# Performance work log

Hardware: AMD Instinct MI355X
Metric: run time of the kernel (lower is better)

The kernel has to match this reference:

```python
import jax, jax.numpy as jnp
import numpy as np

B, C, H, W = 512, 64, 32, 64
NUM_NODE = 128


def setup_inputs() -> dict:
    key = jax.random.key(0)
    ks = jax.random.split(key, 11)
    f = jnp.float32
    def nrm(k, shape, s):
        return jax.random.normal(k, shape, f) * s
    return {
        "x":   jax.random.normal(ks[0], (B, C, H, W), f),
        "w11": nrm(ks[1], (32, 64, 1, 1), 0.1), "b11": nrm(ks[2], (32,), 0.05),
        "w12": nrm(ks[3], (16, 32, 3, 3), 0.1), "b12": nrm(ks[4], (16,), 0.05),
        "w21": nrm(ks[5], (8, 16, 1, 1), 0.1),  "b21": nrm(ks[6], (8,), 0.05),
        "w22": nrm(ks[7], (4, 8, 3, 3), 0.1),   "b22": nrm(ks[8], (4,), 0.05),
        "fcw": nrm(ks[9], (2 * NUM_NODE, 32 * 64 * 4), 0.05),
        "fcb": nrm(ks[10], (2 * NUM_NODE,), 0.05),
    }


def _conv_relu(x, w, b, pad):
    y = jax.lax.conv_general_dilated(
        x, w, window_strides=(1, 1), padding=[(pad, pad), (pad, pad)],
        dimension_numbers=("NCHW", "OIHW", "NCHW"))
    return jax.nn.relu(y + b[None, :, None, None])


def reference(x, w11, b11, w12, b12, w21, b21, w22, b22, fcw, fcb):
    # --- GraphGen3: conv stack -> fc -> n_Sigmoid -> [B, N, 2] ---
    h = _conv_relu(x, w11, b11, 0)
    h = _conv_relu(h, w12, b12, 1)
    h = _conv_relu(h, w21, b21, 0)
    h = _conv_relu(h, w22, b22, 1)          # [B, 4, 32, 64]
    z = h.reshape(h.shape[0], -1) @ fcw.T + fcb  # [B, 2N]
    c01 = jax.nn.sigmoid(3.0 * z).reshape(x.shape[0], -1, 2)  # n_Sigmoid(x, 3)
    # --- get_coord: scale normalized coords to pixel range ---
    Hd, Wd = x.shape[2], x.shape[3]
    coord = c01 * jnp.array([Hd - 1, Wd - 1], x.dtype)  # [B, N, 2]
    # --- th_batch_map_coordinates: clamp, corner gather, bilinear lerp ---
    ch = jnp.clip(coord[..., 0], 0.0, Hd - 1)
    cw = jnp.clip(coord[..., 1], 0.0, Wd - 1)
    h0 = jnp.floor(ch).astype(jnp.int32); h1 = jnp.ceil(ch).astype(jnp.int32)
    w0 = jnp.floor(cw).astype(jnp.int32); w1 = jnp.ceil(cw).astype(jnp.int32)
    bidx = jnp.arange(x.shape[0])[:, None]  # [B, 1]
    def gv(hi, wi):
        return x[bidx, :, hi, wi]           # gather -> [B, N, C]
    v_lt = gv(h0, w0); v_rt = gv(h1, w0)
    v_lb = gv(h0, w1); v_rb = gv(h1, w1)
    oh = (ch - h0.astype(x.dtype))[..., None]
    ow = (cw - w0.astype(x.dtype))[..., None]
    vt = v_lt + oh * (v_rt - v_lt)
    vb = v_lb + oh * (v_rb - v_lb)
    graph_feat = vt + ow * (vb - vt)        # [B, N, C] (matches permute(0,2,1))
    return graph_feat, coord
```

## Files before the change

kernel.cpp:

```cpp
#include <hip/hip_runtime.h>
#include <hip/hip_fp16.h>
#include <cstdint>

#define BATCH 512
#define CIN   64
#define HH    32
#define WW    64
#define HW    2048
#define C1    32
#define C2    16
#define C3    8
#define C4    4
#define NOUT  256
#define KFC   8192
#define NODES 128
#define KS    16
#define GF_SIZE (BATCH * NODES * CIN)

typedef __attribute__((ext_vector_type(8))) short bfrag;
typedef __attribute__((ext_vector_type(4))) float ffrag;

__device__ __forceinline__ ushort bf_trunc(float f) { return (ushort)(__float_as_uint(f) >> 16); }
__device__ __forceinline__ float  bf_truncf(float f) { return __uint_as_float(__float_as_uint(f) & 0xffff0000u); }
__device__ __forceinline__ ushort f2bf(float f) {
  uint32_t u = __float_as_uint(f);
  return (ushort)((u + 0x7fffu + ((u >> 16) & 1u)) >> 16);
}
__device__ __forceinline__ uint32_t pack2(float a, float b) {
  return (uint32_t)f2bf(a) | ((uint32_t)f2bf(b) << 16);
}
__device__ __forceinline__ uint32_t packhi2(float a, float b) {
  return (uint32_t)bf_trunc(a) | ((uint32_t)bf_trunc(b) << 16);
}
__device__ __forceinline__ ushort f2h(float f) { return __half_as_ushort(__float2half_rn(f)); }
__device__ __forceinline__ uint32_t packh2(float a, float b) {
  return (uint32_t)f2h(a) | ((uint32_t)f2h(b) << 16);
}
__device__ __forceinline__ float h2f(uint32_t u) { return __half2float(__ushort_as_half((ushort)u)); }
__device__ __forceinline__ float bf2f(ushort u) { return __uint_as_float(((uint32_t)u) << 16); }

__global__ __launch_bounds__(256) void k_xpose(
    const float* __restrict__ x, ushort* __restrict__ xt)
{
  __shared__ uint32_t tb[256 * 33];
  const int t  = threadIdx.x;
  const int b  = blockIdx.y;
  const int rg = blockIdx.x;
  const float* xp = x + (size_t)b * CIN * HW + rg * 256 + t;
  #pragma unroll
  for (int j = 0; j < 32; ++j) {
    float v0 = xp[(size_t)(2 * j) * HW];
    float v1 = xp[(size_t)(2 * j + 1) * HW];
    tb[t * 33 + j] = pack2(v0, v1);
  }
  __syncthreads();
  ushort* op = xt + ((size_t)b * HW + rg * 256) * CIN;
  #pragma unroll
  for (int k = 0; k < 8; ++k) {
    const int u = k * 256 + t;
    const int p = u >> 3, q = u & 7;
    uint4 v;
    v.x = tb[p * 33 + q * 4 + 0];
    v.y = tb[p * 33 + q * 4 + 1];
    v.z = tb[p * 33 + q * 4 + 2];
    v.w = tb[p * 33 + q * 4 + 3];
    *(uint4*)(op + (size_t)u * 8) = v;
  }
}

__global__ __launch_bounds__(256) void k_conv1234(
    const ushort* __restrict__ xt, const float* __restrict__ w11, const float* __restrict__ b11,
    const float* __restrict__ w12, const float* __restrict__ b12,
    const float* __restrict__ w21, const float* __restrict__ b21,
    const float* __restrict__ w22, const float* __restrict__ b22,
    ushort* __restrict__ h4h, ushort* __restrict__ h4l, int b0)
{
  __shared__ __align__(16) char smem[12 * 66 * 64];
  const int tid = threadIdx.x;
  const int l   = tid & 63;
  const int wv  = tid >> 6;
  const int lr  = l & 15;
  const int lg  = l >> 4;
  const int r0  = blockIdx.x * 8;
  const int bg  = b0 + blockIdx.y;
  const ushort* xtb = xt + (size_t)bg * HW * CIN;

  if (tid < 192) {
    int cell = tid >> 3, q = tid & 7;
    int row = cell >> 1, colb = (cell & 1) ? 65 : 0;
    *(uint2*)(smem + ((row * 66 + colb) << 6) + q * 8) = uint2{0u, 0u};
  }

  bfrag w1h[2][2], w1l[2][2];
  #pragma unroll
  for (int m = 0; m < 2; ++m) {
    #pragma unroll
    for (int ks = 0; ks < 2; ++ks) {
      const float* wp = w11 + (m * 16 + lr) * 64 + ks * 32 + lg * 8;
      #pragma unroll
      for (int e = 0; e < 8; ++e) {
        float v = wp[e];
        w1h[m][ks][e] = (short)bf_trunc(v);
        w1l[m][ks][e] = (short)f2bf(v - bf_truncf(v));
      }
    }
  }
  float bias1[2][4];
  #pragma unroll
  for (int m = 0; m < 2; ++m) {
    #pragma unroll
    for (int r = 0; r < 4; ++r) bias1[m][r] = b11[m * 16 + lg * 4 + r];
  }

  auto ldfrag = [&](int nt, bfrag& f0, bfrag& f1) {
    const int ry = nt >> 2, col0 = (nt & 3) << 4;
    const int y  = r0 - 2 + ry;
    if (y >= 0 && y < HH) {
      const ushort* xp = xtb + (size_t)(y * WW + col0 + lr) * CIN + lg * 8;
      f0 = *(const bfrag*)xp;
      f1 = *(const bfrag*)(xp + 32);
    } else {
      #pragma unroll
      for (int e = 0; e < 8; ++e) { f0[e] = 0; f1[e] = 0; }
    }
  };
  auto comp = [&](int nt, bfrag f0, bfrag f1) {
    const int ry = nt >> 2, col0 = (nt & 3) << 4;
    const int y  = r0 - 2 + ry;
    const bool valid = (y >= 0) && (y < HH);
    const int colb = col0 + 1 + lr;
    ffrag a0 = {0.f, 0.f, 0.f, 0.f}, a1 = {0.f, 0.f, 0.f, 0.f};
    a0 = __builtin_amdgcn_mfma_f32_16x16x32_bf16(w1h[0][0], f0, a0, 0, 0, 0);
    a0 = __builtin_amdgcn_mfma_f32_16x16x32_bf16(w1l[0][0], f0, a0, 0, 0, 0);
    a0 = __builtin_amdgcn_mfma_f32_16x16x32_bf16(w1h[0][1], f1, a0, 0, 0, 0);
    a0 = __builtin_amdgcn_mfma_f32_16x16x32_bf16(w1l[0][1], f1, a0, 0, 0, 0);
    a1 = __builtin_amdgcn_mfma_f32_16x16x32_bf16(w1h[1][0], f0, a1, 0, 0, 0);
    a1 = __builtin_amdgcn_mfma_f32_16x16x32_bf16(w1l[1][0], f0, a1, 0, 0, 0);
    a1 = __builtin_amdgcn_mfma_f32_16x16x32_bf16(w1h[1][1], f1, a1, 0, 0, 0);
    a1 = __builtin_amdgcn_mfma_f32_16x16x32_bf16(w1l[1][1], f1, a1, 0, 0, 0);
    #pragma unroll
    for (int m = 0; m < 2; ++m) {
      uint2 sv;
      if (valid) {
        float v0 = fmaxf((m ? a1[0] : a0[0]) + bias1[m][0], 0.f);
        float v1 = fmaxf((m ? a1[1] : a0[1]) + bias1[m][1], 0.f);
        float v2 = fmaxf((m ? a1[2] : a0[2]) + bias1[m][2], 0.f);
        float v3 = fmaxf((m ? a1[3] : a0[3]) + bias1[m][3], 0.f);
        sv = uint2{pack2(v0, v1), pack2(v2, v3)};
      } else {
        sv = uint2{0u, 0u};
      }
      int chunk = (m * 2 + (lg >> 1)) ^ ((colb >> 1) & 3);
      char* dst = smem + ((ry * 66 + colb) << 6) + (chunk << 4) + (lg & 1) * 8;
      *(uint2*)dst = sv;
    }
  };

  {
    bfrag c0, c1, n0, n1;
    ldfrag(wv * 12 + 0, c0, c1);
    #pragma unroll
    for (int i = 0; i < 12; ++i) {
      if (i < 11) ldfrag(wv * 12 + i + 1, n0, n1);
      comp(wv * 12 + i, c0, c1);
      c0 = n0; c1 = n1;
    }
  }
  __syncthreads();

  bfrag w2h[9], w2l[9];
  #pragma unroll
  for (int t = 0; t < 9; ++t) {
    const float* wp = w12 + lr * 288 + t;
    #pragma unroll
    for (int e = 0; e < 8; ++e) {
      float v = wp[(lg * 8 + e) * 9];
      w2h[t][e] = (short)bf_trunc(v);
      w2l[t][e] = (short)f2bf(v - bf_truncf(v));
    }
  }
  float bias2[4];
  #pragma unroll
  for (int r = 0; r < 4; ++r) bias2[r] = b12[lg * 4 + r];

  uint32_t ph0[10], ph1[10];
  #pragma unroll
  for (int i = 0; i < 10; ++i) {
    const int nt   = wv * 10 + i;
    const int hryo = nt >> 2;
    const int col0 = (nt & 3) << 4;
    ffrag acc = {0.f, 0.f, 0.f, 0.f};
    #pragma unroll
    for (int ky = 0; ky < 3; ++ky) {
      const int row = hryo + ky;
      #pragma unroll
      for (int kx = 0; kx < 3; ++kx) {
        const int colb  = col0 + lr + kx;
        const int chunk = lg ^ ((colb >> 1) & 3);
        const bfrag hv = *(const bfrag*)(smem + ((row * 66 + colb) << 6) + (chunk << 4));
        acc = __builtin_amdgcn_mfma_f32_16x16x32_bf16(w2h[ky * 3 + kx], hv, acc, 0, 0, 0);
        acc = __builtin_amdgcn_mfma_f32_16x16x32_bf16(w2l[ky * 3 + kx], hv, acc, 0, 0, 0);
      }
    }
    ph0[i] = packh2(fmaxf(acc[0] + bias2[0], 0.f), fmaxf(acc[1] + bias2[1], 0.f));
    ph1[i] = packh2(fmaxf(acc[2] + bias2[2], 0.f), fmaxf(acc[3] + bias2[3], 0.f));
  }
  __syncthreads();

  #pragma unroll
  for (int i = 0; i < 10; ++i) {
    const int nt   = wv * 10 + i;
    const int hryo = nt >> 2;
    const int col  = ((nt & 3) << 4) + lr;
    *(uint2*)(smem + ((hryo * 64 + col) << 5) + lg * 8) = uint2{ph0[i], ph1[i]};
  }
  __syncthreads();

  float* h3b = (float*)(smem + 20480);
  for (int p = tid; p < 640; p += 256) {
    const int ry = p >> 6, wc = p & 63;
    const int y  = r0 - 1 + ry;
    float* hd = h3b + (ry * 64 + wc) * 9;
    if (y >= 0 && y < HH) {
      const uint4 ua = *(const uint4*)(smem + ((ry * 64 + wc) << 5));
      const uint4 ub = *(const uint4*)(smem + ((ry * 64 + wc) << 5) + 16);
      uint32_t uw[8] = {ua.x, ua.y, ua.z, ua.w, ub.x, ub.y, ub.z, ub.w};
      float xv[16];
      #pragma unroll
      for (int j = 0; j < 8; ++j) {
        xv[2*j]   = h2f(uw[j] & 0xffffu);
        xv[2*j+1] = h2f(uw[j] >> 16);
      }
      float acc[C3];
      #pragma unroll
      for (int o = 0; o < C3; ++o) acc[o] = b21[o];
      #pragma unroll
      for (int c = 0; c < 16; ++c) {
        float v = xv[c];
        #pragma unroll
        for (int o = 0; o < C3; ++o)
          acc[o] = fmaf(v, w21[o * 16 + c], acc[o]);
      }
      #pragma unroll
      for (int c = 0; c < C3; ++c) hd[c] = fmaxf(acc[c], 0.f);
    } else {
      #pragma unroll
      for (int c = 0; c < C3; ++c) hd[c] = 0.f;
    }
  }
  __syncthreads();

  for (int p = tid; p < 512; p += 256) {
    const int yl = p >> 6, wc = p & 63;
    float acc[C4] = {b22[0], b22[1], b22[2], b22[3]};
    #pragma unroll
    for (int ky = 0; ky < 3; ++ky) {
      #pragma unroll
      for (int kx = 0; kx < 3; ++kx) {
        const int wcc = wc + kx - 1;
        if (wcc < 0 || wcc >= WW) continue;
        const float* hb = h3b + ((yl + ky) * 64 + wcc) * 9;
        const int tap = ky * 3 + kx;
        #pragma unroll
        for (int c = 0; c < C3; ++c) {
          float v = hb[c];
          #pragma unroll
          for (int o = 0; o < C4; ++o)
            acc[o] = fmaf(v, w22[(o * 8 + c) * 9 + tap], acc[o]);
        }
      }
    }
    const size_t base = (size_t)blockIdx.y * KFC + (r0 + yl) * WW + wc;
    #pragma unroll
    for (int o = 0; o < C4; ++o) {
      float v = fmaxf(acc[o], 0.f);
      h4h[base + (size_t)o * HW] = bf_trunc(v);
      h4l[base + (size_t)o * HW] = f2bf(v - bf_truncf(v));
    }
  }
}

__global__ __launch_bounds__(256) void k_cvt_fcw(
    const float* __restrict__ w, ushort* __restrict__ hi, ushort* __restrict__ lo)
{
  const int i = (blockIdx.x * 256 + threadIdx.x) * 8;
  const float4 a = *(const float4*)(w + i);
  const float4 b = *(const float4*)(w + i + 4);
  uint4 hv, lv;
  hv.x = packhi2(a.x, a.y); hv.y = packhi2(a.z, a.w);
  hv.z = packhi2(b.x, b.y); hv.w = packhi2(b.z, b.w);
  lv.x = pack2(a.x - bf_truncf(a.x), a.y - bf_truncf(a.y));
  lv.y = pack2(a.z - bf_truncf(a.z), a.w - bf_truncf(a.w));
  lv.z = pack2(b.x - bf_truncf(b.x), b.y - bf_truncf(b.y));
  lv.w = pack2(b.z - bf_truncf(b.z), b.w - bf_truncf(b.w));
  *(uint4*)(hi + i) = hv;
  *(uint4*)(lo + i) = lv;
}

__global__ __launch_bounds__(256) void k_fc(
    const ushort* __restrict__ Ahp, const ushort* __restrict__ Alp,
    const ushort* __restrict__ Bhp, const ushort* __restrict__ Blp,
    float* __restrict__ zpart, int cb)
{
  const int tid = threadIdx.x;
  const int l   = tid & 63;
  const int wv  = tid >> 6;
  const int lr  = l & 15;
  const int lg  = l >> 4;
  const int m0  = blockIdx.x * 64 + (wv >> 1) * 32;
  const int n0  = blockIdx.y * 64 + (wv & 1) * 32;
  const int k0  = blockIdx.z * (KFC / KS);

  int mrow[2], nrow[2];
  #pragma unroll
  for (int t = 0; t < 2; ++t) {
    int m = m0 + t * 16 + lr;
    mrow[t] = m < cb ? m : cb - 1;
    nrow[t] = n0 + t * 16 + lr;
  }
  ffrag acc[2][2] = {};

  #pragma unroll 1
  for (int kc = 0; kc < (KFC / KS) / 32; ++kc) {
    const int k = k0 + kc * 32 + lg * 8;
    bfrag ah[2], al[2], bh[2], bl[2];
    #pragma unroll
    for (int t = 0; t < 2; ++t) {
      ah[t] = *(const bfrag*)(Ahp + (size_t)mrow[t] * KFC + k);
      al[t] = *(const bfrag*)(Alp + (size_t)mrow[t] * KFC + k);
      bh[t] = *(const bfrag*)(Bhp + (size_t)nrow[t] * KFC + k);
      bl[t] = *(const bfrag*)(Blp + (size_t)nrow[t] * KFC + k);
    }
    #pragma unroll
    for (int mt = 0; mt < 2; ++mt) {
      #pragma unroll
      for (int nt = 0; nt < 2; ++nt) {
        acc[mt][nt] = __builtin_amdgcn_mfma_f32_16x16x32_bf16(ah[mt], bh[nt], acc[mt][nt], 0, 0, 0);
        acc[mt][nt] = __builtin_amdgcn_mfma_f32_16x16x32_bf16(ah[mt], bl[nt], acc[mt][nt], 0, 0, 0);
        acc[mt][nt] = __builtin_amdgcn_mfma_f32_16x16x32_bf16(al[mt], bh[nt], acc[mt][nt], 0, 0, 0);
      }
    }
  }

  #pragma unroll
  for (int mt = 0; mt < 2; ++mt) {
    #pragma unroll
    for (int r = 0; r < 4; ++r) {
      const int m = m0 + mt * 16 + lg * 4 + r;
      if (m < cb) {
        #pragma unroll
        for (int nt = 0; nt < 2; ++nt)
          zpart[((size_t)blockIdx.z * cb + m) * NOUT + n0 + nt * 16 + lr] = acc[mt][nt][r];
      }
    }
  }
}

__global__ __launch_bounds__(256) void k_gather(
    const ushort* __restrict__ xt, const float* __restrict__ zpart,
    const float* __restrict__ fcb, float* __restrict__ out, int cb, int b0)
{
  const int bid = blockIdx.x;
  int bl, g;
  if ((cb & 7) == 0) {
    const int xcd = bid & 7;
    const int j   = bid >> 3;
    g  = j & 31;
    bl = (j >> 5) * 8 + xcd;
  } else {
    bl = bid >> 5;
    g  = bid & 31;
  }
  const int node = g * 4 + (threadIdx.x >> 6);
  const int l    = threadIdx.x & 63;
  const int bg   = b0 + bl;

  float val = 0.f;
  if (l < 2 * KS) {
    const int kb = l >> 1, comp = l & 1;
    val = zpart[((size_t)kb * cb + bl) * NOUT + node * 2 + comp];
  }
  #pragma unroll
  for (int off = 2; off < 2 * KS; off <<= 1) val += __shfl_xor(val, off);
  const float z0 = __shfl(val, 0) + fcb[node * 2 + 0];
  const float z1 = __shfl(val, 1) + fcb[node * 2 + 1];
  const float ch = 31.f / (1.f + __expf(-3.f * z0));
  const float cw = 63.f / (1.f + __expf(-3.f * z1));

  if (l < 2)
    out[GF_SIZE + (((size_t)bg * NODES + node) << 1) + l] = l ? cw : ch;

  const float chv = fminf(fmaxf(ch, 0.f), 31.f);
  const float cwv = fminf(fmaxf(cw, 0.f), 63.f);
  const float fh = floorf(chv), fw = floorf(cwv);
  const int h0 = (int)fh, h1i = (int)ceilf(chv);
  const int w0 = (int)fw, w1i = (int)ceilf(cwv);
  const float oh = chv - fh, ow = cwv - fw;
  const ushort* xbp = xt + (size_t)bg * HW * CIN + l;
  const float v_lt = bf2f(xbp[(size_t)(h0 * WW + w0) * CIN]);
  const float v_rt = bf2f(xbp[(size_t)(h1i * WW + w0) * CIN]);
  const float v_lb = bf2f(xbp[(size_t)(h0 * WW + w1i) * CIN]);
  const float v_rb = bf2f(xbp[(size_t)(h1i * WW + w1i) * CIN]);
  const float vt = v_lt + oh * (v_rt - v_lt);
  const float vb = v_lb + oh * (v_rb - v_lb);
  out[((size_t)bg * NODES + node) * CIN + l] = vt + ow * (vb - vt);
}

extern "C" void kernel_launch(void* const* d_in, const int* in_sizes, int n_in,
                              void* d_out, int out_size, void* d_ws, size_t ws_size,
                              hipStream_t stream)
{
  (void)in_sizes; (void)n_in; (void)out_size;
  const float* x   = (const float*)d_in[0];
  const float* w11 = (const float*)d_in[1];
  const float* b11 = (const float*)d_in[2];
  const float* w12 = (const float*)d_in[3];
  const float* b12 = (const float*)d_in[4];
  const float* w21 = (const float*)d_in[5];
  const float* b21 = (const float*)d_in[6];
  const float* w22 = (const float*)d_in[7];
  const float* b22 = (const float*)d_in[8];
  const float* fcw = (const float*)d_in[9];
  const float* fcb = (const float*)d_in[10];
  float* out = (float*)d_out;
  char* wsb  = (char*)d_ws;

  const size_t xtBytes = (size_t)BATCH * HW * CIN * 2;
  const size_t perB    = 16384 + 16384 + (size_t)KS * NOUT * 4;
  const size_t fixed   = xtBytes + 2 * 4194304;
  size_t avail = ws_size > fixed ? ws_size - fixed : perB;
  size_t cbmax = avail / perB;
  int CB = (int)(cbmax < (size_t)BATCH ? cbmax : (size_t)BATCH);
  if (CB < 1) CB = 1;

  char* p = wsb;
  ushort* xtv  = (ushort*)p;  p += xtBytes;
  ushort* h4h  = (ushort*)p;  p += (size_t)CB * 16384;
  ushort* h4l  = (ushort*)p;  p += (size_t)CB * 16384;
  float*  zpv  = (float*)p;   p += (size_t)CB * KS * NOUT * 4;
  ushort* fcwh = (ushort*)p;  p += 4194304;
  ushort* fcwl = (ushort*)p;

  k_cvt_fcw<<<dim3(NOUT * KFC / (256 * 8)), 256, 0, stream>>>(fcw, fcwh, fcwl);
  k_xpose<<<dim3(8, BATCH), 256, 0, stream>>>(x, xtv);

  for (int b0 = 0; b0 < BATCH; b0 += CB) {
    const int cb = (BATCH - b0 < CB) ? (BATCH - b0) : CB;
    k_conv1234<<<dim3(4, cb), 256, 0, stream>>>(xtv, w11, b11, w12, b12,
                                                w21, b21, w22, b22, h4h, h4l, b0);
    k_fc<<<dim3((cb + 63) / 64, 4, KS), 256, 0, stream>>>(h4h, h4l, fcwh, fcwl, zpv, cb);
    k_gather<<<dim3(cb * 32), 256, 0, stream>>>(xtv, zpv, fcb, out, cb, b0);
  }
}
```

Before: 225.2 us.

## Process whole image per 1024-thread block to eliminate conv halo recomputation

```diff
diff --git a/kernel.cpp b/kernel.cpp
--- a/kernel.cpp
+++ b/kernel.cpp
@@ -68,27 +68,30 @@
   }
 }
 
-__global__ __launch_bounds__(256) void k_conv1234(
+__global__ __launch_bounds__(1024) void k_conv1234(
     const ushort* __restrict__ xt, const float* __restrict__ w11, const float* __restrict__ b11,
     const float* __restrict__ w12, const float* __restrict__ b12,
     const float* __restrict__ w21, const float* __restrict__ b21,
     const float* __restrict__ w22, const float* __restrict__ b22,
     ushort* __restrict__ h4h, ushort* __restrict__ h4l, int b0)
 {
-  __shared__ __align__(16) char smem[12 * 66 * 64];
+  __shared__ __align__(16) char smem[141568];
   const int tid = threadIdx.x;
   const int l   = tid & 63;
   const int wv  = tid >> 6;
   const int lr  = l & 15;
   const int lg  = l >> 4;
-  const int r0  = blockIdx.x * 8;
-  const int bg  = b0 + blockIdx.y;
+  const int bg  = b0 + blockIdx.x;
   const ushort* xtb = xt + (size_t)bg * HW * CIN;
 
-  if (tid < 192) {
-    int cell = tid >> 3, q = tid & 7;
-    int row = cell >> 1, colb = (cell & 1) ? 65 : 0;
-    *(uint2*)(smem + ((row * 66 + colb) << 6) + q * 8) = uint2{0u, 0u};
+  if (tid < 264) {
+    int row = tid >> 3, rem = tid & 7;
+    int colb = (rem < 4) ? 0 : 65, q = rem & 3;
+    *(uint4*)(smem + ((row * 66 + colb) << 6) + q * 16) = uint4{0u, 0u, 0u, 0u};
+  } else if (tid < 528) {
+    int idx = tid - 264;
+    int col = idx >> 2, q = idx & 3;
+    *(uint4*)(smem + ((32 * 66 + col) << 6) + q * 16) = uint4{0u, 0u, 0u, 0u};
   }
 
   bfrag w1h[2][2], w1l[2][2];
@@ -114,20 +117,12 @@
 
   auto ldfrag = [&](int nt, bfrag& f0, bfrag& f1) {
     const int ry = nt >> 2, col0 = (nt & 3) << 4;
-    const int y  = r0 - 2 + ry;
-    if (y >= 0 && y < HH) {
-      const ushort* xp = xtb + (size_t)(y * WW + col0 + lr) * CIN + lg * 8;
-      f0 = *(const bfrag*)xp;
-      f1 = *(const bfrag*)(xp + 32);
-    } else {
-      #pragma unroll
-      for (int e = 0; e < 8; ++e) { f0[e] = 0; f1[e] = 0; }
-    }
+    const ushort* xp = xtb + (size_t)(ry * WW + col0 + lr) * CIN + lg * 8;
+    f0 = *(const bfrag*)xp;
+    f1 = *(const bfrag*)(xp + 32);
   };
   auto comp = [&](int nt, bfrag f0, bfrag f1) {
     const int ry = nt >> 2, col0 = (nt & 3) << 4;
-    const int y  = r0 - 2 + ry;
-    const bool valid = (y >= 0) && (y < HH);
     const int colb = col0 + 1 + lr;
     ffrag a0 = {0.f, 0.f, 0.f, 0.f}, a1 = {0.f, 0.f, 0.f, 0.f};
     a0 = __builtin_amdgcn_mfma_f32_16x16x32_bf16(w1h[0][0], f0, a0, 0, 0, 0);
@@ -140,29 +135,23 @@
     a1 = __builtin_amdgcn_mfma_f32_16x16x32_bf16(w1l[1][1], f1, a1, 0, 0, 0);
     #pragma unroll
     for (int m = 0; m < 2; ++m) {
-      uint2 sv;
-      if (valid) {
-        float v0 = fmaxf((m ? a1[0] : a0[0]) + bias1[m][0], 0.f);
-        float v1 = fmaxf((m ? a1[1] : a0[1]) + bias1[m][1], 0.f);
-        float v2 = fmaxf((m ? a1[2] : a0[2]) + bias1[m][2], 0.f);
-        float v3 = fmaxf((m ? a1[3] : a0[3]) + bias1[m][3], 0.f);
-        sv = uint2{pack2(v0, v1), pack2(v2, v3)};
-      } else {
-        sv = uint2{0u, 0u};
-      }
+      float v0 = fmaxf((m ? a1[0] : a0[0]) + bias1[m][0], 0.f);
+      float v1 = fmaxf((m ? a1[1] : a0[1]) + bias1[m][1], 0.f);
+      float v2 = fmaxf((m ? a1[2] : a0[2]) + bias1[m][2], 0.f);
+      float v3 = fmaxf((m ? a1[3] : a0[3]) + bias1[m][3], 0.f);
       int chunk = (m * 2 + (lg >> 1)) ^ ((colb >> 1) & 3);
       char* dst = smem + ((ry * 66 + colb) << 6) + (chunk << 4) + (lg & 1) * 8;
-      *(uint2*)dst = sv;
+      *(uint2*)dst = uint2{pack2(v0, v1), pack2(v2, v3)};
     }
   };
 
   {
     bfrag c0, c1, n0, n1;
-    ldfrag(wv * 12 + 0, c0, c1);
-    #pragma unroll
-    for (int i = 0; i < 12; ++i) {
-      if (i < 11) ldfrag(wv * 12 + i + 1, n0, n1);
-      comp(wv * 12 + i, c0, c1);
+    ldfrag(wv * 8 + 0, c0, c1);
+    #pragma unroll
+    for (int i = 0; i < 8; ++i) {
+      if (i < 7) ldfrag(wv * 8 + i + 1, n0, n1);
+      comp(wv * 8 + i, c0, c1);
       c0 = n0; c1 = n1;
     }
   }
@@ -183,16 +172,17 @@
   #pragma unroll
   for (int r = 0; r < 4; ++r) bias2[r] = b12[lg * 4 + r];
 
-  uint32_t ph0[10], ph1[10];
-  #pragma unroll
-  for (int i = 0; i < 10; ++i) {
-    const int nt   = wv * 10 + i;
-    const int hryo = nt >> 2;
+  uint32_t ph0[8], ph1[8];
+  #pragma unroll
+  for (int i = 0; i < 8; ++i) {
+    const int nt   = wv * 8 + i;
+    const int hy   = nt >> 2;
     const int col0 = (nt & 3) << 4;
     ffrag acc = {0.f, 0.f, 0.f, 0.f};
     #pragma unroll
     for (int ky = 0; ky < 3; ++ky) {
-      const int row = hryo + ky;
+      const int yv  = hy - 1 + ky;
+      const int row = ((unsigned)yv < 32u) ? yv : 32;
       #pragma unroll
       for (int kx = 0; kx < 3; ++kx) {
         const int colb  = col0 + lr + kx;
@@ -208,58 +198,62 @@
   __syncthreads();
 
   #pragma unroll
-  for (int i = 0; i < 10; ++i) {
-    const int nt   = wv * 10 + i;
-    const int hryo = nt >> 2;
-    const int col  = ((nt & 3) << 4) + lr;
-    *(uint2*)(smem + ((hryo * 64 + col) << 5) + lg * 8) = uint2{ph0[i], ph1[i]};
+  for (int i = 0; i < 8; ++i) {
+    const int nt  = wv * 8 + i;
+    const int hy  = nt >> 2;
+    const int col = ((nt & 3) << 4) + lr;
+    *(uint2*)(smem + ((hy * 64 + col) << 5) + lg * 8) = uint2{ph0[i], ph1[i]};
   }
   __syncthreads();
 
-  float* h3b = (float*)(smem + 20480);
-  for (int p = tid; p < 640; p += 256) {
+  float* h3b = (float*)(smem + 65536);
+  if (tid < 576) {
+    const int px = tid / 9, c = tid - px * 9;
+    h3b[(32 * 64 + px) * 9 + c] = 0.f;
+  }
+  #pragma unroll
+  for (int it = 0; it < 2; ++it) {
+    const int p  = it * 1024 + tid;
     const int ry = p >> 6, wc = p & 63;
-    const int y  = r0 - 1 + ry;
+    const uint4 ua = *(const uint4*)(smem + ((ry * 64 + wc) << 5));
+    const uint4 ub = *(const uint4*)(smem + ((ry * 64 + wc) << 5) + 16);
+    uint32_t uw[8] = {ua.x, ua.y, ua.z, ua.w, ub.x, ub.y, ub.z, ub.w};
+    float xv[16];
+    #pragma unroll
+    for (int j = 0; j < 8; ++j) {
+      xv[2*j]   = h2f(uw[j] & 0xffffu);
+      xv[2*j+1] = h2f(uw[j] >> 16);
+    }
+    float acc[C3];
+    #pragma unroll
+    for (int o = 0; o < C3; ++o) acc[o] = b21[o];
+    #pragma unroll
+    for (int c = 0; c < 16; ++c) {
+      float v = xv[c];
+      #pragma unroll
+      for (int o = 0; o < C3; ++o)
+        acc[o] = fmaf(v, w21[o * 16 + c], acc[o]);
+    }
     float* hd = h3b + (ry * 64 + wc) * 9;
-    if (y >= 0 && y < HH) {
-      const uint4 ua = *(const uint4*)(smem + ((ry * 64 + wc) << 5));
-      const uint4 ub = *(const uint4*)(smem + ((ry * 64 + wc) << 5) + 16);
-      uint32_t uw[8] = {ua.x, ua.y, ua.z, ua.w, ub.x, ub.y, ub.z, ub.w};
-      float xv[16];
-      #pragma unroll
-      for (int j = 0; j < 8; ++j) {
-        xv[2*j]   = h2f(uw[j] & 0xffffu);
-        xv[2*j+1] = h2f(uw[j] >> 16);
-      }
-      float acc[C3];
-      #pragma unroll
-      for (int o = 0; o < C3; ++o) acc[o] = b21[o];
-      #pragma unroll
-      for (int c = 0; c < 16; ++c) {
-        float v = xv[c];
-        #pragma unroll
-        for (int o = 0; o < C3; ++o)
-          acc[o] = fmaf(v, w21[o * 16 + c], acc[o]);
-      }
-      #pragma unroll
-      for (int c = 0; c < C3; ++c) hd[c] = fmaxf(acc[c], 0.f);
-    } else {
-      #pragma unroll
-      for (int c = 0; c < C3; ++c) hd[c] = 0.f;
-    }
+    #pragma unroll
+    for (int c = 0; c < C3; ++c) hd[c] = fmaxf(acc[c], 0.f);
   }
   __syncthreads();
 
-  for (int p = tid; p < 512; p += 256) {
+  #pragma unroll
+  for (int it = 0; it < 2; ++it) {
+    const int p  = it * 1024 + tid;
     const int yl = p >> 6, wc = p & 63;
     float acc[C4] = {b22[0], b22[1], b22[2], b22[3]};
     #pragma unroll
     for (int ky = 0; ky < 3; ++ky) {
+      const int yv  = yl - 1 + ky;
+      const int row = ((unsigned)yv < 32u) ? yv : 32;
       #pragma unroll
       for (int kx = 0; kx < 3; ++kx) {
         const int wcc = wc + kx - 1;
         if (wcc < 0 || wcc >= WW) continue;
-        const float* hb = h3b + ((yl + ky) * 64 + wcc) * 9;
+        const float* hb = h3b + (row * 64 + wcc) * 9;
         const int tap = ky * 3 + kx;
         #pragma unroll
         for (int c = 0; c < C3; ++c) {
@@ -270,7 +264,7 @@
         }
       }
     }
-    const size_t base = (size_t)blockIdx.y * KFC + (r0 + yl) * WW + wc;
+    const size_t base = (size_t)blockIdx.x * KFC + yl * WW + wc;
     #pragma unroll
     for (int o = 0; o < C4; ++o) {
       float v = fmaxf(acc[o], 0.f);
@@ -446,8 +440,8 @@
 
   for (int b0 = 0; b0 < BATCH; b0 += CB) {
     const int cb = (BATCH - b0 < CB) ? (BATCH - b0) : CB;
-    k_conv1234<<<dim3(4, cb), 256, 0, stream>>>(xtv, w11, b11, w12, b12,
-                                                w21, b21, w22, b22, h4h, h4l, b0);
+    k_conv1234<<<dim3(cb), 1024, 0, stream>>>(xtv, w11, b11, w12, b12,
+                                              w21, b21, w22, b22, h4h, h4l, b0);
     k_fc<<<dim3((cb + 63) / 64, 4, KS), 256, 0, stream>>>(h4h, h4l, fcwh, fcwl, zpv, cb);
     k_gather<<<dim3(cb * 32), 256, 0, stream>>>(xtv, zpv, fcb, out, cb, b0);
   }
```

Result: slower. 275.0 us (+22.1%).

## Move 1x1 conv into transpose kernel and merge fcw conversion launch

Applied to the files above, without the earlier changes.

```diff
diff --git a/kernel.cpp b/kernel.cpp
--- a/kernel.cpp
+++ b/kernel.cpp
@@ -39,38 +39,117 @@
 __device__ __forceinline__ float h2f(uint32_t u) { return __half2float(__ushort_as_half((ushort)u)); }
 __device__ __forceinline__ float bf2f(ushort u) { return __uint_as_float(((uint32_t)u) << 16); }
 
-__global__ __launch_bounds__(256) void k_xpose(
-    const float* __restrict__ x, ushort* __restrict__ xt)
+__device__ __forceinline__ bfrag ld_frag4(const uint32_t* tp) {
+  union { uint32_t u[4]; bfrag b; } c;
+  c.u[0] = tp[0]; c.u[1] = tp[1]; c.u[2] = tp[2]; c.u[3] = tp[3];
+  return c.b;
+}
+
+__global__ __launch_bounds__(256) void k_front(
+    const float* __restrict__ x, const float* __restrict__ w11, const float* __restrict__ b11,
+    const float* __restrict__ fcw, ushort* __restrict__ fcwh, ushort* __restrict__ fcwl,
+    ushort* __restrict__ xt, ushort* __restrict__ h1g)
 {
+  if (blockIdx.y >= BATCH) {
+    const int chunk = (blockIdx.y - BATCH) * 8 + blockIdx.x;
+    const int i = (chunk * 256 + threadIdx.x) * 8;
+    const float4 a = *(const float4*)(fcw + i);
+    const float4 b = *(const float4*)(fcw + i + 4);
+    uint4 hv, lv;
+    hv.x = packhi2(a.x, a.y); hv.y = packhi2(a.z, a.w);
+    hv.z = packhi2(b.x, b.y); hv.w = packhi2(b.z, b.w);
+    lv.x = pack2(a.x - bf_truncf(a.x), a.y - bf_truncf(a.y));
+    lv.y = pack2(a.z - bf_truncf(a.z), a.w - bf_truncf(a.w));
+    lv.z = pack2(b.x - bf_truncf(b.x), b.y - bf_truncf(b.y));
+    lv.w = pack2(b.z - bf_truncf(b.z), b.w - bf_truncf(b.w));
+    *(uint4*)(fcwh + i) = hv;
+    *(uint4*)(fcwl + i) = lv;
+    return;
+  }
+
   __shared__ uint32_t tb[256 * 33];
   const int t  = threadIdx.x;
   const int b  = blockIdx.y;
   const int rg = blockIdx.x;
-  const float* xp = x + (size_t)b * CIN * HW + rg * 256 + t;
-  #pragma unroll
-  for (int j = 0; j < 32; ++j) {
-    float v0 = xp[(size_t)(2 * j) * HW];
-    float v1 = xp[(size_t)(2 * j + 1) * HW];
-    tb[t * 33 + j] = pack2(v0, v1);
-  }
-  __syncthreads();
-  ushort* op = xt + ((size_t)b * HW + rg * 256) * CIN;
-  #pragma unroll
-  for (int k = 0; k < 8; ++k) {
-    const int u = k * 256 + t;
-    const int p = u >> 3, q = u & 7;
-    uint4 v;
-    v.x = tb[p * 33 + q * 4 + 0];
-    v.y = tb[p * 33 + q * 4 + 1];
-    v.z = tb[p * 33 + q * 4 + 2];
-    v.w = tb[p * 33 + q * 4 + 3];
-    *(uint4*)(op + (size_t)u * 8) = v;
-  }
-}
-
-__global__ __launch_bounds__(256) void k_conv1234(
-    const ushort* __restrict__ xt, const float* __restrict__ w11, const float* __restrict__ b11,
-    const float* __restrict__ w12, const float* __restrict__ b12,
+  {
+    const float* xp = x + (size_t)b * CIN * HW + rg * 256 + t;
+    #pragma unroll
+    for (int j = 0; j < 32; ++j) {
+      float v0 = xp[(size_t)(2 * j) * HW];
+      float v1 = xp[(size_t)(2 * j + 1) * HW];
+      tb[t * 33 + j] = pack2(v0, v1);
+    }
+  }
+  __syncthreads();
+
+  {
+    ushort* op = xt + ((size_t)b * HW + rg * 256) * CIN;
+    #pragma unroll
+    for (int k = 0; k < 8; ++k) {
+      const int u = k * 256 + t;
+      const int p = u >> 3, q = u & 7;
+      uint4 v;
+      v.x = tb[p * 33 + q * 4 + 0];
+      v.y = tb[p * 33 + q * 4 + 1];
+      v.z = tb[p * 33 + q * 4 + 2];
+      v.w = tb[p * 33 + q * 4 + 3];
+      *(uint4*)(op + (size_t)u * 8) = v;
+    }
+  }
+
+  const int l  = t & 63;
+  const int wv = t >> 6;
+  const int lr = l & 15;
+  const int lg = l >> 4;
+  bfrag w1h[2][2], w1l[2][2];
+  #pragma unroll
+  for (int m = 0; m < 2; ++m) {
+    #pragma unroll
+    for (int ks = 0; ks < 2; ++ks) {
+      const float* wp = w11 + (m * 16 + lr) * 64 + ks * 32 + lg * 8;
+      #pragma unroll
+      for (int e = 0; e < 8; ++e) {
+        float v = wp[e];
+        w1h[m][ks][e] = (short)bf_trunc(v);
+        w1l[m][ks][e] = (short)f2bf(v - bf_truncf(v));
+      }
+    }
+  }
+  float bias1[2][4];
+  #pragma unroll
+  for (int m = 0; m < 2; ++m) {
+    #pragma unroll
+    for (int r = 0; r < 4; ++r) bias1[m][r] = b11[m * 16 + lg * 4 + r];
+  }
+
+  #pragma unroll
+  for (int i = 0; i < 4; ++i) {
+    const int pxl = (wv * 4 + i) * 16 + lr;
+    const bfrag f0 = ld_frag4(&tb[pxl * 33 + lg * 4]);
+    const bfrag f1 = ld_frag4(&tb[pxl * 33 + 16 + lg * 4]);
+    ffrag a0 = {0.f, 0.f, 0.f, 0.f}, a1 = {0.f, 0.f, 0.f, 0.f};
+    a0 = __builtin_amdgcn_mfma_f32_16x16x32_bf16(w1h[0][0], f0, a0, 0, 0, 0);
+    a0 = __builtin_amdgcn_mfma_f32_16x16x32_bf16(w1l[0][0], f0, a0, 0, 0, 0);
+    a0 = __builtin_amdgcn_mfma_f32_16x16x32_bf16(w1h[0][1], f1, a0, 0, 0, 0);
+    a0 = __builtin_amdgcn_mfma_f32_16x16x32_bf16(w1l[0][1], f1, a0, 0, 0, 0);
+    a1 = __builtin_amdgcn_mfma_f32_16x16x32_bf16(w1h[1][0], f0, a1, 0, 0, 0);
+    a1 = __builtin_amdgcn_mfma_f32_16x16x32_bf16(w1l[1][0], f0, a1, 0, 0, 0);
+    a1 = __builtin_amdgcn_mfma_f32_16x16x32_bf16(w1h[1][1], f1, a1, 0, 0, 0);
+    a1 = __builtin_amdgcn_mfma_f32_16x16x32_bf16(w1l[1][1], f1, a1, 0, 0, 0);
+    ushort* hp = h1g + ((size_t)b * HW + rg * 256 + pxl) * C1;
+    #pragma unroll
+    for (int m = 0; m < 2; ++m) {
+      float v0 = fmaxf((m ? a1[0] : a0[0]) + bias1[m][0], 0.f);
+      float v1 = fmaxf((m ? a1[1] : a0[1]) + bias1[m][1], 0.f);
+      float v2 = fmaxf((m ? a1[2] : a0[2]) + bias1[m][2], 0.f);
+      float v3 = fmaxf((m ? a1[3] : a0[3]) + bias1[m][3], 0.f);
+      *(uint2*)(hp + m * 16 + lg * 4) = uint2{pack2(v0, v1), pack2(v2, v3)};
+    }
+  }
+}
+
+__global__ __launch_bounds__(256) void k_conv234(
+    const ushort* __restrict__ h1g, const float* __restrict__ w12, const float* __restrict__ b12,
     const float* __restrict__ w21, const float* __restrict__ b21,
     const float* __restrict__ w22, const float* __restrict__ b22,
     ushort* __restrict__ h4h, ushort* __restrict__ h4l, int b0)
@@ -83,87 +162,25 @@
   const int lg  = l >> 4;
   const int r0  = blockIdx.x * 8;
   const int bg  = b0 + blockIdx.y;
-  const ushort* xtb = xt + (size_t)bg * HW * CIN;
 
   if (tid < 192) {
-    int cell = tid >> 3, q = tid & 7;
-    int row = cell >> 1, colb = (cell & 1) ? 65 : 0;
-    *(uint2*)(smem + ((row * 66 + colb) << 6) + q * 8) = uint2{0u, 0u};
-  }
-
-  bfrag w1h[2][2], w1l[2][2];
-  #pragma unroll
-  for (int m = 0; m < 2; ++m) {
-    #pragma unroll
-    for (int ks = 0; ks < 2; ++ks) {
-      const float* wp = w11 + (m * 16 + lr) * 64 + ks * 32 + lg * 8;
-      #pragma unroll
-      for (int e = 0; e < 8; ++e) {
-        float v = wp[e];
-        w1h[m][ks][e] = (short)bf_trunc(v);
-        w1l[m][ks][e] = (short)f2bf(v - bf_truncf(v));
-      }
-    }
-  }
-  float bias1[2][4];
-  #pragma unroll
-  for (int m = 0; m < 2; ++m) {
-    #pragma unroll
-    for (int r = 0; r < 4; ++r) bias1[m][r] = b11[m * 16 + lg * 4 + r];
-  }
-
-  auto ldfrag = [&](int nt, bfrag& f0, bfrag& f1) {
-    const int ry = nt >> 2, col0 = (nt & 3) << 4;
-    const int y  = r0 - 2 + ry;
-    if (y >= 0 && y < HH) {
-      const ushort* xp = xtb + (size_t)(y * WW + col0 + lr) * CIN + lg * 8;
-      f0 = *(const bfrag*)xp;
-      f1 = *(const bfrag*)(xp + 32);
-    } else {
-      #pragma unroll
-      for (int e = 0; e < 8; ++e) { f0[e] = 0; f1[e] = 0; }
-    }
-  };
-  auto comp = [&](int nt, bfrag f0, bfrag f1) {
-    const int ry = nt >> 2, col0 = (nt & 3) << 4;
-    const int y  = r0 - 2 + ry;
-    const bool valid = (y >= 0) && (y < HH);
-    const int colb = col0 + 1 + lr;
-    ffrag a0 = {0.f, 0.f, 0.f, 0.f}, a1 = {0.f, 0.f, 0.f, 0.f};
-    a0 = __builtin_amdgcn_mfma_f32_16x16x32_bf16(w1h[0][0], f0, a0, 0, 0, 0);
-    a0 = __builtin_amdgcn_mfma_f32_16x16x32_bf16(w1l[0][0], f0, a0, 0, 0, 0);
-    a0 = __builtin_amdgcn_mfma_f32_16x16x32_bf16(w1h[0][1], f1, a0, 0, 0, 0);
-    a0 = __builtin_amdgcn_mfma_f32_16x16x32_bf16(w1l[0][1], f1, a0, 0, 0, 0);
-    a1 = __builtin_amdgcn_mfma_f32_16x16x32_bf16(w1h[1][0], f0, a1, 0, 0, 0);
-    a1 = __builtin_amdgcn_mfma_f32_16x16x32_bf16(w1l[1][0], f0, a1, 0, 0, 0);
-    a1 = __builtin_amdgcn_mfma_f32_16x16x32_bf16(w1h[1][1], f1, a1, 0, 0, 0);
-    a1 = __builtin_amdgcn_mfma_f32_16x16x32_bf16(w1l[1][1], f1, a1, 0, 0, 0);
-    #pragma unroll
-    for (int m = 0; m < 2; ++m) {
-      uint2 sv;
-      if (valid) {
-        float v0 = fmaxf((m ? a1[0] : a0[0]) + bias1[m][0], 0.f);
-        float v1 = fmaxf((m ? a1[1] : a0[1]) + bias1[m][1], 0.f);
-        float v2 = fmaxf((m ? a1[2] : a0[2]) + bias1[m][2], 0.f);
-        float v3 = fmaxf((m ? a1[3] : a0[3]) + bias1[m][3], 0.f);
-        sv = uint2{pack2(v0, v1), pack2(v2, v3)};
-      } else {
-        sv = uint2{0u, 0u};
-      }
-      int chunk = (m * 2 + (lg >> 1)) ^ ((colb >> 1) & 3);
-      char* dst = smem + ((ry * 66 + colb) << 6) + (chunk << 4) + (lg & 1) * 8;
-      *(uint2*)dst = sv;
-    }
-  };
+    int row = tid >> 4, half = (tid >> 3) & 1, q = tid & 7;
+    int cell = row * 66 + (half ? 65 : 0);
+    *(uint2*)(smem + (cell << 6) + q * 8) = uint2{0u, 0u};
+  }
+  __syncthreads();
 
   {
-    bfrag c0, c1, n0, n1;
-    ldfrag(wv * 12 + 0, c0, c1);
-    #pragma unroll
-    for (int i = 0; i < 12; ++i) {
-      if (i < 11) ldfrag(wv * 12 + i + 1, n0, n1);
-      comp(wv * 12 + i, c0, c1);
-      c0 = n0; c1 = n1;
+    const int px = tid >> 2, q = tid & 3;
+    const int colb  = px + 1;
+    const int chunk = q ^ ((colb >> 1) & 3);
+    #pragma unroll
+    for (int ry = 0; ry < 12; ++ry) {
+      const int y = r0 - 2 + ry;
+      uint4 v = uint4{0u, 0u, 0u, 0u};
+      if (y >= 0 && y < HH)
+        v = *(const uint4*)(h1g + ((size_t)bg * HW + y * WW + px) * C1 + q * 8);
+      *(uint4*)(smem + ((ry * 66 + colb) << 6) + (chunk << 4)) = v;
     }
   }
   __syncthreads();
@@ -251,7 +268,7 @@
   __syncthreads();
 
   for (int p = tid; p < 512; p += 256) {
-    const int yl = p >> 6, wc = p & 63;
+    const int yl = p >> 6, wc = p & 63, ry = yl + 1;
     float acc[C4] = {b22[0], b22[1], b22[2], b22[3]};
     #pragma unroll
     for (int ky = 0; ky < 3; ++ky) {
@@ -259,7 +276,7 @@
       for (int kx = 0; kx < 3; ++kx) {
         const int wcc = wc + kx - 1;
         if (wcc < 0 || wcc >= WW) continue;
-        const float* hb = h3b + ((yl + ky) * 64 + wcc) * 9;
+        const float* hb = h3b + ((ry + ky - 1) * 64 + wcc) * 9;
         const int tap = ky * 3 + kx;
         #pragma unroll
         for (int c = 0; c < C3; ++c) {
@@ -278,23 +295,6 @@
       h4l[base + (size_t)o * HW] = f2bf(v - bf_truncf(v));
     }
   }
-}
-
-__global__ __launch_bounds__(256) void k_cvt_fcw(
-    const float* __restrict__ w, ushort* __restrict__ hi, ushort* __restrict__ lo)
-{
-  const int i = (blockIdx.x * 256 + threadIdx.x) * 8;
-  const float4 a = *(const float4*)(w + i);
-  const float4 b = *(const float4*)(w + i + 4);
-  uint4 hv, lv;
-  hv.x = packhi2(a.x, a.y); hv.y = packhi2(a.z, a.w);
-  hv.z = packhi2(b.x, b.y); hv.w = packhi2(b.z, b.w);
-  lv.x = pack2(a.x - bf_truncf(a.x), a.y - bf_truncf(a.y));
-  lv.y = pack2(a.z - bf_truncf(a.z), a.w - bf_truncf(a.w));
-  lv.z = pack2(b.x - bf_truncf(b.x), b.y - bf_truncf(b.y));
-  lv.w = pack2(b.z - bf_truncf(b.z), b.w - bf_truncf(b.w));
-  *(uint4*)(hi + i) = hv;
-  *(uint4*)(lo + i) = lv;
 }
 
 __global__ __launch_bounds__(256) void k_fc(
@@ -426,8 +426,9 @@
   char* wsb  = (char*)d_ws;
 
   const size_t xtBytes = (size_t)BATCH * HW * CIN * 2;
+  const size_t h1Bytes = (size_t)BATCH * HW * C1 * 2;
   const size_t perB    = 16384 + 16384 + (size_t)KS * NOUT * 4;
-  const size_t fixed   = xtBytes + 2 * 4194304;
+  const size_t fixed   = xtBytes + h1Bytes + 2 * 4194304;
   size_t avail = ws_size > fixed ? ws_size - fixed : perB;
   size_t cbmax = avail / perB;
   int CB = (int)(cbmax < (size_t)BATCH ? cbmax : (size_t)BATCH);
@@ -435,19 +436,20 @@
 
   char* p = wsb;
   ushort* xtv  = (ushort*)p;  p += xtBytes;
+  ushort* h1v  = (ushort*)p;  p += h1Bytes;
   ushort* h4h  = (ushort*)p;  p += (size_t)CB * 16384;
   ushort* h4l  = (ushort*)p;  p += (size_t)CB * 16384;
   float*  zpv  = (float*)p;   p += (size_t)CB * KS * NOUT * 4;
   ushort* fcwh = (ushort*)p;  p += 4194304;
   ushort* fcwl = (ushort*)p;
 
-  k_cvt_fcw<<<dim3(NOUT * KFC / (256 * 8)), 256, 0, stream>>>(fcw, fcwh, fcwl);
-  k_xpose<<<dim3(8, BATCH), 256, 0, stream>>>(x, xtv);
+  k_front<<<dim3(8, BATCH + 128), 256, 0, stream>>>(x, w11, b11, fcw, fcwh, fcwl,
+                                                    xtv, h1v);
 
   for (int b0 = 0; b0 < BATCH; b0 += CB) {
     const int cb = (BATCH - b0 < CB) ? (BATCH - b0) : CB;
-    k_conv1234<<<dim3(4, cb), 256, 0, stream>>>(xtv, w11, b11, w12, b12,
-                                                w21, b21, w22, b22, h4h, h4l, b0);
+    k_conv234<<<dim3(4, cb), 256, 0, stream>>>(h1v, w12, b12, w21, b21, w22, b22,
+                                               h4h, h4l, b0);
     k_fc<<<dim3((cb + 63) / 64, 4, KS), 256, 0, stream>>>(h4h, h4l, fcwh, fcwl, zpv, cb);
     k_gather<<<dim3(cb * 32), 256, 0, stream>>>(xtv, zpv, fcb, out, cb, b0);
   }
```

Result: no change. 223.9 us (-0.6%).
